# Performance work log

Measured on AMD Instinct MI355X. Metric: run time of the kernel, lower is better.

Reference implementation:

```python
import jax, jax.numpy as jnp
import numpy as np

NUM_NODES = 100000
EMBED_DIM = 256
NUM_EDGES = 16384
TOTAL = 524288  # total flattened hyperedge membership entries


def setup_inputs() -> dict:
    key = jax.random.key(0)
    k1, k2, k3 = jax.random.split(key, 3)
    node_embeddings = jax.random.normal(k1, (NUM_NODES, EMBED_DIM), dtype=jnp.float32)
    node_indices = jax.random.randint(k2, (TOTAL,), 0, NUM_NODES, dtype=jnp.int64)
    segment_ids = jnp.sort(jax.random.randint(k3, (TOTAL,), 0, NUM_EDGES, dtype=jnp.int64))
    return {"node_embeddings": node_embeddings, "node_indices": node_indices, "segment_ids": segment_ids}


def reference(node_embeddings, node_indices, segment_ids):
    # Gather member-node embeddings: [TOTAL, D]
    gathered = node_embeddings[node_indices]
    # Segmented sum over hyperedges: [NUM_EDGES, D]
    seg_sum = jax.ops.segment_sum(gathered, segment_ids, num_segments=NUM_EDGES)
    # Per-hyperedge member counts for the mean; guard empty segments.
    counts = jax.ops.segment_sum(jnp.ones((gathered.shape[0],), dtype=gathered.dtype),
                                 segment_ids, num_segments=NUM_EDGES)
    counts = jnp.maximum(counts, 1.0)
    return seg_sum / counts[:, None]
```

## Files before the change

kernel.cpp:

```cpp
#include <hip/hip_runtime.h>


#define EMBED_DIM 256
#define NUM_EDGES 16384
#define TOTAL_MEM 524288

__global__ __launch_bounds__(256) void seg_bounds_kernel(
    const int* __restrict__ seg_ids,
    int*       __restrict__ seg_start)
{
    const int i = blockIdx.x * blockDim.x + threadIdx.x;
    if (i >= TOTAL_MEM) return;
    const int cur  = seg_ids[i];
    const int prev = (i == 0) ? -1 : seg_ids[i - 1];
    for (int s = prev + 1; s <= cur; ++s) seg_start[s] = i;
    if (i == TOTAL_MEM - 1) {
        for (int s = cur + 1; s <= NUM_EDGES; ++s) seg_start[s] = TOTAL_MEM;
    }
}

__global__ __launch_bounds__(256) void hyperedge_agg_kernel(
    const float* __restrict__ emb,
    const int*   __restrict__ node_idx,
    const int*   __restrict__ seg_start,
    float*       __restrict__ out)
{
    const int wave = threadIdx.x >> 6;
    const int lane = threadIdx.x & 63;
    const int seg  = blockIdx.x * 4 + wave;
    if (seg >= NUM_EDGES) return;

    const int start = seg_start[seg];
    const int end   = seg_start[seg + 1];

    float4 acc = make_float4(0.f, 0.f, 0.f, 0.f);

    int i = start;
    while (i < end) {
        const int batch = min(end - i, 64);
        const int my = (lane < batch) ? node_idx[i + lane] : 0;

        for (int j = 0; j < batch; j += 8) {
            const int m = min(batch - j, 8);
            int ns[8];
            #pragma unroll
            for (int t = 0; t < 8; ++t) ns[t] = __shfl(my, j + t);
            float4 v[8];
            #pragma unroll
            for (int t = 0; t < 8; ++t)
                if (t < m)
                    v[t] = ((const float4*)(emb + (size_t)ns[t] * EMBED_DIM))[lane];
            #pragma unroll
            for (int t = 0; t < 8; ++t)
                if (t < m) {
                    acc.x += v[t].x; acc.y += v[t].y;
                    acc.z += v[t].z; acc.w += v[t].w;
                }
        }
        i += batch;
    }

    const float cnt = (end > start) ? (float)(end - start) : 1.0f;
    acc.x /= cnt; acc.y /= cnt; acc.z /= cnt; acc.w /= cnt;

    ((float4*)(out + (size_t)seg * EMBED_DIM))[lane] = acc;
}

__global__ __launch_bounds__(256) void hyperedge_agg_bsearch_kernel(
    const float* __restrict__ emb,
    const int*   __restrict__ node_idx,
    const int*   __restrict__ seg_ids,
    float*       __restrict__ out)
{
    const int wave = threadIdx.x >> 6;
    const int lane = threadIdx.x & 63;
    const int seg  = blockIdx.x * 4 + wave;
    if (seg >= NUM_EDGES) return;

    int lo = 0, hi = TOTAL_MEM;
    while (lo < hi) {
        int mid = (lo + hi) >> 1;
        if (seg_ids[mid] < seg) lo = mid + 1; else hi = mid;
    }
    const int start = lo;
    hi = TOTAL_MEM;
    while (lo < hi) {
        int mid = (lo + hi) >> 1;
        if (seg_ids[mid] < seg + 1) lo = mid + 1; else hi = mid;
    }
    const int end = lo;

    float4 acc = make_float4(0.f, 0.f, 0.f, 0.f);
    for (int i = start; i < end; ++i) {
        const int n = node_idx[i];
        float4 v = ((const float4*)(emb + (size_t)n * EMBED_DIM))[lane];
        acc.x += v.x; acc.y += v.y; acc.z += v.z; acc.w += v.w;
    }
    const float cnt = (end > start) ? (float)(end - start) : 1.0f;
    acc.x /= cnt; acc.y /= cnt; acc.z /= cnt; acc.w /= cnt;
    ((float4*)(out + (size_t)seg * EMBED_DIM))[lane] = acc;
}

extern "C" void kernel_launch(void* const* d_in, const int* in_sizes, int n_in,
                              void* d_out, int out_size, void* d_ws, size_t ws_size,
                              hipStream_t stream) {
    const float* emb      = (const float*)d_in[0];
    const int*   node_idx = (const int*)d_in[1];
    const int*   seg_ids  = (const int*)d_in[2];
    float*       out      = (float*)d_out;

    const size_t bounds_bytes = (size_t)(NUM_EDGES + 1) * sizeof(int);
    if (ws_size >= bounds_bytes) {
        int* seg_start = (int*)d_ws;
        seg_bounds_kernel<<<(TOTAL_MEM + 255) / 256, 256, 0, stream>>>(seg_ids, seg_start);
        hyperedge_agg_kernel<<<NUM_EDGES / 4, 256, 0, stream>>>(emb, node_idx, seg_start, out);
    } else {
        hyperedge_agg_bsearch_kernel<<<NUM_EDGES / 4, 256, 0, stream>>>(emb, node_idx, seg_ids, out);
    }
}
```

Measured before the change: 205.2 us.

## Convert embedding table to fp16 in workspace and gather half-width rows

Adds a pass that converts the full fp32 node-embedding table to fp16 in the workspace on every call. The aggregation kernel then gathers 8-byte fp16 chunks per lane and accumulates in fp32, halving the bytes read by the random gather. The cost is an extra full-table read and half-size write each call, plus fp16 rounding of the inputs, and the path only runs when the workspace holds the fp16 table. The fp32 kernel also moves the shuffle inside its load loop.

```diff
diff --git a/kernel.cpp b/kernel.cpp
--- a/kernel.cpp
+++ b/kernel.cpp
@@ -1,9 +1,35 @@
 #include <hip/hip_runtime.h>
+#include <hip/hip_fp16.h>
 
 
 #define EMBED_DIM 256
 #define NUM_EDGES 16384
 #define TOTAL_MEM 524288
+#define NUM_NODES 100000
+
+#define TAB16_BYTES ((size_t)NUM_NODES * EMBED_DIM * 2)
+#define BOUNDS_BYTES ((size_t)(NUM_EDGES + 1) * sizeof(int))
+
+__global__ __launch_bounds__(256) void convert_f32_to_f16_kernel(
+    const float4* __restrict__ in,
+    uint4*        __restrict__ out)
+{
+    const int j = blockIdx.x * blockDim.x + threadIdx.x;
+    const int n_out = NUM_NODES * (EMBED_DIM / 8);
+    if (j >= n_out) return;
+    float4 a = in[2 * j];
+    float4 b = in[2 * j + 1];
+    __half2 h0 = __floats2half2_rn(a.x, a.y);
+    __half2 h1 = __floats2half2_rn(a.z, a.w);
+    __half2 h2 = __floats2half2_rn(b.x, b.y);
+    __half2 h3 = __floats2half2_rn(b.z, b.w);
+    uint4 o;
+    o.x = *reinterpret_cast<unsigned int*>(&h0);
+    o.y = *reinterpret_cast<unsigned int*>(&h1);
+    o.z = *reinterpret_cast<unsigned int*>(&h2);
+    o.w = *reinterpret_cast<unsigned int*>(&h3);
+    out[j] = o;
+}
 
 __global__ __launch_bounds__(256) void seg_bounds_kernel(
     const int* __restrict__ seg_ids,
@@ -19,6 +45,57 @@
     }
 }
 
+__global__ __launch_bounds__(256) void hyperedge_agg_f16_kernel(
+    const uint2* __restrict__ tab,
+    const int*   __restrict__ node_idx,
+    const int*   __restrict__ seg_start,
+    float*       __restrict__ out)
+{
+    const int wave = threadIdx.x >> 6;
+    const int lane = threadIdx.x & 63;
+    const int seg  = blockIdx.x * 4 + wave;
+    if (seg >= NUM_EDGES) return;
+
+    const int start = seg_start[seg];
+    const int end   = seg_start[seg + 1];
+
+    float4 acc = make_float4(0.f, 0.f, 0.f, 0.f);
+
+    int i = start;
+    while (i < end) {
+        const int batch = min(end - i, 64);
+        const int my = (lane < batch) ? node_idx[i + lane] : 0;
+
+        for (int j = 0; j < batch; j += 8) {
+            const int m = min(batch - j, 8);
+            uint2 v[8];
+            #pragma unroll
+            for (int t = 0; t < 8; ++t)
+                if (t < m) {
+                    const int n = __shfl(my, j + t);
+                    v[t] = tab[(size_t)n * (EMBED_DIM / 4) + lane];
+                }
+            #pragma unroll
+            for (int t = 0; t < 8; ++t)
+                if (t < m) {
+                    __half2 h0 = *reinterpret_cast<__half2*>(&v[t].x);
+                    __half2 h1 = *reinterpret_cast<__half2*>(&v[t].y);
+                    float2 f0 = __half22float2(h0);
+                    float2 f1 = __half22float2(h1);
+                    acc.x += f0.x; acc.y += f0.y;
+                    acc.z += f1.x; acc.w += f1.y;
+                }
+        }
+        i += batch;
+    }
+
+    const float cnt = (end > start) ? (float)(end - start) : 1.0f;
+    acc.x /= cnt; acc.y /= cnt; acc.z /= cnt; acc.w /= cnt;
+
+    ((float4*)(out + (size_t)seg * EMBED_DIM))[lane] = acc;
+}
+
+
 __global__ __launch_bounds__(256) void hyperedge_agg_kernel(
     const float* __restrict__ emb,
     const int*   __restrict__ node_idx,
@@ -34,22 +111,19 @@
     const int end   = seg_start[seg + 1];
 
     float4 acc = make_float4(0.f, 0.f, 0.f, 0.f);
-
     int i = start;
     while (i < end) {
         const int batch = min(end - i, 64);
         const int my = (lane < batch) ? node_idx[i + lane] : 0;
-
         for (int j = 0; j < batch; j += 8) {
             const int m = min(batch - j, 8);
-            int ns[8];
-            #pragma unroll
-            for (int t = 0; t < 8; ++t) ns[t] = __shfl(my, j + t);
             float4 v[8];
             #pragma unroll
             for (int t = 0; t < 8; ++t)
-                if (t < m)
-                    v[t] = ((const float4*)(emb + (size_t)ns[t] * EMBED_DIM))[lane];
+                if (t < m) {
+                    const int n = __shfl(my, j + t);
+                    v[t] = ((const float4*)(emb + (size_t)n * EMBED_DIM))[lane];
+                }
             #pragma unroll
             for (int t = 0; t < 8; ++t)
                 if (t < m) {
@@ -59,10 +133,8 @@
         }
         i += batch;
     }
-
     const float cnt = (end > start) ? (float)(end - start) : 1.0f;
     acc.x /= cnt; acc.y /= cnt; acc.z /= cnt; acc.w /= cnt;
-
     ((float4*)(out + (size_t)seg * EMBED_DIM))[lane] = acc;
 }
 
@@ -109,8 +181,17 @@
     const int*   seg_ids  = (const int*)d_in[2];
     float*       out      = (float*)d_out;
 
-    const size_t bounds_bytes = (size_t)(NUM_EDGES + 1) * sizeof(int);
-    if (ws_size >= bounds_bytes) {
+    if (ws_size >= TAB16_BYTES + BOUNDS_BYTES) {
+        uint4* tab16     = (uint4*)d_ws;
+        int*   seg_start = (int*)((char*)d_ws + TAB16_BYTES);
+
+        const int n_out4 = NUM_NODES * (EMBED_DIM / 8);
+        convert_f32_to_f16_kernel<<<(n_out4 + 255) / 256, 256, 0, stream>>>(
+            (const float4*)emb, tab16);
+        seg_bounds_kernel<<<(TOTAL_MEM + 255) / 256, 256, 0, stream>>>(seg_ids, seg_start);
+        hyperedge_agg_f16_kernel<<<NUM_EDGES / 4, 256, 0, stream>>>(
+            (const uint2*)tab16, node_idx, seg_start, out);
+    } else if (ws_size >= BOUNDS_BYTES) {
         int* seg_start = (int*)d_ws;
         seg_bounds_kernel<<<(TOTAL_MEM + 255) / 256, 256, 0, stream>>>(seg_ids, seg_start);
         hyperedge_agg_kernel<<<NUM_EDGES / 4, 256, 0, stream>>>(emb, node_idx, seg_start, out);
```

Result: no change. 208.5 us (+1.6%).
